# Optimization experiments

Measured on AMD Instinct MI355X. Metric: run time of the kernel, lower is better.

## Reference

```python
import jax, jax.numpy as jnp
import numpy as np

B, T, C = 4, 2048, 1024
N_HEAD = 16
HEAD_DIM = C // N_HEAD


def setup_inputs() -> dict:
    key = jax.random.key(0)
    k1, k2, k3 = jax.random.split(key, 3)
    x = jax.random.normal(k1, (B, T, C), dtype=jnp.float32)
    # torch Linear(n_embd, 3*n_embd, bias=False): weight [out,in]; store transposed [in,out]
    w_qkv = jax.random.normal(k2, (C, 3 * C), dtype=jnp.float32) * (1.0 / np.sqrt(C))
    w_proj = jax.random.normal(k3, (C, C), dtype=jnp.float32) * (1.0 / np.sqrt(C))
    return {"x": x, "w_qkv": w_qkv, "w_proj": w_proj}


def reference(x, w_qkv, w_proj):
    Bb, Tt, Cc = x.shape
    qkv = x @ w_qkv  # [B,T,3C]
    q, k, v = jnp.split(qkv, 3, axis=2)
    # [B,T,H,D] -> [B,H,T,D]
    def heads(t):
        return t.reshape(Bb, Tt, N_HEAD, HEAD_DIM).transpose(0, 2, 1, 3)
    q, k, v = heads(q), heads(k), heads(v)
    att = jnp.einsum("bhqd,bhkd->bhqk", q, k) / jnp.sqrt(jnp.float32(HEAD_DIM))
    causal = jnp.tril(jnp.ones((Tt, Tt), dtype=bool))
    att = jnp.where(causal, att, -jnp.inf)
    att = jax.nn.softmax(att, axis=-1)
    y = jnp.einsum("bhqk,bhkd->bhqd", att, v)  # [B,H,T,D]
    y = y.transpose(0, 2, 1, 3).reshape(Bb, Tt, Cc)
    return y @ w_proj
```

## Files before the change

### kernel.cpp

```cpp
#include <hip/hip_runtime.h>
#include <hip/hip_bf16.h>

typedef unsigned short u16;
typedef __bf16 bf16x8 __attribute__((ext_vector_type(8)));
typedef float f32x4 __attribute__((ext_vector_type(4)));
typedef float f32x16 __attribute__((ext_vector_type(16)));
typedef unsigned short u16x8 __attribute__((ext_vector_type(8)));
typedef unsigned short u16x4 __attribute__((ext_vector_type(4)));
typedef unsigned int u32x4 __attribute__((ext_vector_type(4)));

__device__ __forceinline__ u16 f2bf(float f) {
  unsigned u = __builtin_bit_cast(unsigned, f);
  u += 0x7FFFu + ((u >> 16) & 1u);
  return (u16)(u >> 16);
}

__device__ __forceinline__ unsigned cvt_pk_bf16(float lo, float hi_) {
  unsigned r;
  asm("v_cvt_pk_bf16_f32 %0, %1, %2" : "=v"(r) : "v"(lo), "v"(hi_));
  return r;
}

#define GLD16(gp, lp)                                                          \
  __builtin_amdgcn_global_load_lds(                                            \
      (const __attribute__((address_space(1))) void*)(gp),                     \
      (__attribute__((address_space(3))) void*)(lp), 16, 0, 0)


__global__ __launch_bounds__(256) void cast_f32_bf16(
    const float* __restrict__ in, u16* __restrict__ out, int n4) {
  int i = blockIdx.x * 256 + threadIdx.x;
  if (i >= n4) return;
  float4 v = ((const float4*)in)[i];
  u16x4 o = {f2bf(v.x), f2bf(v.y), f2bf(v.z), f2bf(v.w)};
  *(u16x4*)(out + (size_t)i * 4) = o;
}

__global__ __launch_bounds__(256) void transpose_cast(
    const float* __restrict__ in, u16* __restrict__ out, int R, int C) {
  __shared__ float t[32][33];
  int c0 = blockIdx.x * 32, r0 = blockIdx.y * 32;
  int tx = threadIdx.x, ty = threadIdx.y;
#pragma unroll
  for (int k = 0; k < 4; ++k)
    t[ty + 8 * k][tx] = in[(size_t)(r0 + ty + 8 * k) * C + c0 + tx];
  __syncthreads();
#pragma unroll
  for (int k = 0; k < 4; ++k)
    out[(size_t)(c0 + ty + 8 * k) * R + r0 + tx] = f2bf(t[tx][ty + 8 * k]);
}


template <int EPI>
__global__ __launch_bounds__(256) void gemm_bt(
    const u16* __restrict__ A, const u16* __restrict__ Bt, int K,
    u16* __restrict__ Qd, u16* __restrict__ Kd, u16* __restrict__ Vd,
    float* __restrict__ Od, int N) {
  __shared__ u16 As[128 * 64];
  __shared__ u16 Bs[128 * 64];
  int tid = threadIdx.x;
  int l = tid & 63, w = tid >> 6;
  int wr = w >> 1, wc = w & 1;
  int lr = l & 15, lg = l >> 4;
  int nwg = (int)gridDim.x;
  int bid = (int)blockIdx.x;
  int wg = (bid & 7) * (nwg >> 3) + (bid >> 3);
  int nx = N >> 7;
  int m0 = (wg / nx) * 128, n0 = (wg % nx) * 128;

  f32x4 acc[4][4];
  f32x4 z4 = {0.f, 0.f, 0.f, 0.f};
#pragma unroll
  for (int mi = 0; mi < 4; ++mi)
#pragma unroll
    for (int ni = 0; ni < 4; ++ni) acc[mi][ni] = z4;

  for (int kt = 0; kt < K; kt += 64) {
#pragma unroll
    for (int it = 0; it < 4; ++it) {
      int q = it * 256 + tid;
      int r = q >> 3, s = q & 7;
      int sw = (s ^ (r & 7)) << 3;
      GLD16(A + (size_t)(m0 + r) * K + kt + sw, As + it * 2048 + w * 512);
      GLD16(Bt + (size_t)(n0 + r) * K + kt + sw, Bs + it * 2048 + w * 512);
    }
    __syncthreads();

#pragma unroll
    for (int ks2 = 0; ks2 < 2; ++ks2) {
      bf16x8 af[4], bfv[4];
#pragma unroll
      for (int mi = 0; mi < 4; ++mi) {
        int row = wr * 64 + mi * 16 + lr;
        af[mi] = *(const bf16x8*)&As[row * 64 + (((ks2 * 4 + lg) ^ (row & 7)) << 3)];
      }
#pragma unroll
      for (int ni = 0; ni < 4; ++ni) {
        int col = wc * 64 + ni * 16 + lr;
        bfv[ni] = *(const bf16x8*)&Bs[col * 64 + (((ks2 * 4 + lg) ^ (col & 7)) << 3)];
      }
#pragma unroll
      for (int mi = 0; mi < 4; ++mi)
#pragma unroll
        for (int ni = 0; ni < 4; ++ni)
          acc[mi][ni] = __builtin_amdgcn_mfma_f32_16x16x32_bf16(
              af[mi], bfv[ni], acc[mi][ni], 0, 0, 0);
    }
    __syncthreads();
  }

  if (EPI == 0) {
    int s_blk = n0 >> 10;
    u16* dst = (s_blk == 0) ? Qd : ((s_blk == 1) ? Kd : Vd);
#pragma unroll
    for (int mi = 0; mi < 4; ++mi)
#pragma unroll
      for (int ni = 0; ni < 4; ++ni)
#pragma unroll
        for (int i = 0; i < 4; ++i) {
          int m = m0 + wr * 64 + mi * 16 + lg * 4 + i;
          int n = n0 + wc * 64 + ni * 16 + lr;
          int b = m >> 11, t = m & 2047;
          int c = n & 1023, h = c >> 6, d = c & 63;
          dst[((size_t)(b * 16 + h) * 2048 + t) * 64 + d] = f2bf(acc[mi][ni][i]);
        }
  } else {
#pragma unroll
    for (int mi = 0; mi < 4; ++mi)
#pragma unroll
      for (int ni = 0; ni < 4; ++ni)
#pragma unroll
        for (int i = 0; i < 4; ++i) {
          int m = m0 + wr * 64 + mi * 16 + lg * 4 + i;
          int n = n0 + wc * 64 + ni * 16 + lr;
          Od[(size_t)m * N + n] = acc[mi][ni][i];
        }
  }
}


__global__ __launch_bounds__(128, 3) void attn_fwd(
    const u16* __restrict__ Qg, const u16* __restrict__ Kg,
    const u16* __restrict__ Vg, u16* __restrict__ Yg) {
  __shared__ u16 Ks[2][64 * 64];
  __shared__ u16 Vt[64 * 64];

  int tid = threadIdx.x;
  int l = tid & 63, w = tid >> 6;
  int l31 = l & 31, hi = l >> 5, l7 = l & 7;
  int bid = blockIdx.x;
  int qt = 31 - (bid >> 6);
  int bh = bid & 63;
  const u16* Qb = Qg + (size_t)bh * 131072;
  const u16* Kb = Kg + (size_t)bh * 131072;
  const u16* Vb = Vg + (size_t)bh * 131072;
  int b = bh >> 4, h = bh & 15;

  int t8 = tid >> 3, dq = tid & 7;
  int q0w = qt * 64 + w * 32;
  int jn = qt;

  bf16x8 qreg[4];
#pragma unroll
  for (int ds = 0; ds < 4; ++ds)
    qreg[ds] =
        *(const bf16x8*)(Qb + (size_t)(q0w + l31) * 64 + ds * 16 + hi * 8);

  f32x16 o_acc[2];
#pragma unroll
  for (int dt = 0; dt < 2; ++dt)
#pragma unroll
    for (int r = 0; r < 16; ++r) o_acc[dt][r] = 0.f;
  float m_run = -3e38f, l_run = 0.f;

  u16x8 va[2], vb[2];
#pragma unroll
  for (int it = 0; it < 4; ++it) {
    int r = it * 16 + t8;
    GLD16(Kb + (size_t)r * 64 + ((dq ^ (r & 7)) << 3),
          &Ks[0][it * 1024 + w * 512]);
  }
#pragma unroll
  for (int it = 0; it < 2; ++it) {
    int rr = it * 16 + t8;
    va[it] = *(const u16x8*)(Vb + (size_t)(2 * rr) * 64 + dq * 8);
    vb[it] = *(const u16x8*)(Vb + (size_t)(2 * rr + 1) * 64 + dq * 8);
  }

  for (int j = 0; j <= jn; ++j) {
    int kv0 = j * 64;
    const u16* ksb = Ks[j & 1];
#pragma unroll
    for (int it = 0; it < 2; ++it) {
      int rr = it * 16 + t8;
      int rr2 = (rr & ~6) | ((rr & 2) << 1) | ((rr & 4) >> 1);
#pragma unroll
      for (int jj = 0; jj < 8; ++jj) {
        int d = dq * 8 + jj;
        unsigned wv = (unsigned)va[it][jj] | ((unsigned)vb[it][jj] << 16);
        *(unsigned*)(Vt + d * 64 + (((rr2 >> 2) ^ jj ^ dq) << 3) +
                     ((rr2 & 3) << 1)) = wv;
      }
    }
    __syncthreads();

    if (j < jn) {
      int kv1 = kv0 + 64;
#pragma unroll
      for (int it = 0; it < 4; ++it) {
        int r = it * 16 + t8;
        GLD16(Kb + (size_t)(kv1 + r) * 64 + ((dq ^ (r & 7)) << 3),
              &Ks[(j + 1) & 1][it * 1024 + w * 512]);
      }
#pragma unroll
      for (int it = 0; it < 2; ++it) {
        int rr = it * 16 + t8;
        va[it] = *(const u16x8*)(Vb + (size_t)(kv1 + 2 * rr) * 64 + dq * 8);
        vb[it] = *(const u16x8*)(Vb + (size_t)(kv1 + 2 * rr + 1) * 64 + dq * 8);
      }
    }

    {
      int qg = q0w + l31;
      bf16x8 kf[2][4];
#pragma unroll
      for (int kt = 0; kt < 2; ++kt)
#pragma unroll
        for (int ds = 0; ds < 4; ++ds)
          kf[kt][ds] = *(const bf16x8*)&ksb[(32 * kt + l31) * 64 +
                                            (((2 * ds + hi) ^ l7) << 3)];
      f32x16 sa[2];
      __builtin_amdgcn_s_setprio(1);
#pragma unroll
      for (int kt = 0; kt < 2; ++kt) {
        f32x16 acc;
#pragma unroll
        for (int r = 0; r < 16; ++r) acc[r] = 0.f;
#pragma unroll
        for (int ds = 0; ds < 4; ++ds)
          acc = __builtin_amdgcn_mfma_f32_32x32x16_bf16(kf[kt][ds], qreg[ds],
                                                        acc, 0, 0, 0);
        sa[kt] = acc;
      }
      __builtin_amdgcn_s_setprio(0);

      float mloc = -3e38f;
      if (kv0 + 63 > q0w) {
#pragma unroll
        for (int kt = 0; kt < 2; ++kt)
#pragma unroll
          for (int r = 0; r < 16; ++r) {
            int kg = kv0 + kt * 32 + ((r & 3) + 8 * (r >> 2) + 4 * hi);
            float v = sa[kt][r];
            v = (kg <= qg) ? v : -8e30f;
            sa[kt][r] = v;
            mloc = fmaxf(mloc, v);
          }
      } else {
#pragma unroll
        for (int kt = 0; kt < 2; ++kt)
#pragma unroll
          for (int r = 0; r < 16; ++r) mloc = fmaxf(mloc, sa[kt][r]);
      }
      float mx = fmaxf(mloc, __shfl_xor(mloc, 32)) * 0.125f;
      if (!__all(mx <= m_run + 8.f)) {
        float mn = fmaxf(m_run, mx);
        float fsc = __expf(m_run - mn);
        m_run = mn;
        l_run *= fsc;
#pragma unroll
        for (int r = 0; r < 16; ++r) {
          float fv = __shfl(fsc, (r & 3) + 8 * (r >> 2) + 4 * hi + 32 * hi);
          o_acc[0][r] *= fv;
          o_acc[1][r] *= fv;
        }
      }
      float mm = m_run * 1.44269504f;
      float lloc = 0.f;
#pragma unroll
      for (int kt = 0; kt < 2; ++kt)
#pragma unroll
        for (int r = 0; r < 16; ++r) {
          float p = exp2f(__builtin_fmaf(sa[kt][r], 0.18033688f, -mm));
          sa[kt][r] = p;
          lloc += p;
        }
      l_run += lloc;
      unsigned pk0[8], pk1[8];
#pragma unroll
      for (int m = 0; m < 8; ++m) {
        pk0[m] = cvt_pk_bf16(sa[0][2 * m], sa[0][2 * m + 1]);
        pk1[m] = cvt_pk_bf16(sa[1][2 * m], sa[1][2 * m + 1]);
      }
      bf16x8 vf[2][4];
#pragma unroll
      for (int dt = 0; dt < 2; ++dt)
#pragma unroll
        for (int ks = 0; ks < 4; ++ks) {
          int d = 32 * dt + l31;
          int ch = ((2 * ks + hi) ^ (d & 7) ^ ((d >> 3) & 7)) & 7;
          vf[dt][ks] = *(const bf16x8*)&Vt[d * 64 + (ch << 3)];
        }
#pragma unroll
      for (int ks = 0; ks < 4; ++ks) {
        int c0 = 4 * (ks & 1);
        u32x4 fa;
        fa.x = (ks < 2) ? pk0[c0] : pk1[c0];
        fa.y = (ks < 2) ? pk0[c0 + 1] : pk1[c0 + 1];
        fa.z = (ks < 2) ? pk0[c0 + 2] : pk1[c0 + 2];
        fa.w = (ks < 2) ? pk0[c0 + 3] : pk1[c0 + 3];
        bf16x8 paf = __builtin_bit_cast(bf16x8, fa);
        __builtin_amdgcn_s_setprio(1);
#pragma unroll
        for (int dt = 0; dt < 2; ++dt)
          o_acc[dt] = __builtin_amdgcn_mfma_f32_32x32x16_bf16(
              paf, vf[dt][ks], o_acc[dt], 0, 0, 0);
        __builtin_amdgcn_s_setprio(0);
      }
    }
    __builtin_amdgcn_sched_barrier(0);
    __builtin_amdgcn_s_barrier();
    __builtin_amdgcn_sched_barrier(0);
  }

  l_run += __shfl_xor(l_run, 32);

#pragma unroll
  for (int r = 0; r < 16; ++r) {
    int crow = (r & 3) + 8 * (r >> 2) + 4 * hi;
    float li = __shfl(l_run, crow + 32 * hi);
    float inv = 1.f / li;
    int q = q0w + crow;
#pragma unroll
    for (int dt = 0; dt < 2; ++dt) {
      float y = o_acc[dt][r] * inv;
      Yg[(size_t)(b * 2048 + q) * 1024 + h * 64 + dt * 32 + l31] = f2bf(y);
    }
  }
}


extern "C" void kernel_launch(void* const* d_in, const int* in_sizes, int n_in,
                              void* d_out, int out_size, void* d_ws, size_t ws_size,
                              hipStream_t stream) {
  const float* x = (const float*)d_in[0];
  const float* w_qkv = (const float*)d_in[1];
  const float* w_proj = (const float*)d_in[2];
  float* out = (float*)d_out;
  u16* ws = (u16*)d_ws;

  u16* xb = ws;
  u16* wq = xb + 8388608;
  u16* wp = wq + 3145728;
  u16* Qb = wp + 1048576;
  u16* Kb = Qb + 8388608;
  u16* Vb = Kb + 8388608;
  u16* Yb = xb;

  cast_f32_bf16<<<8192, 256, 0, stream>>>(x, xb, 2097152);
  transpose_cast<<<dim3(96, 32), dim3(32, 8), 0, stream>>>(w_qkv, wq, 1024, 3072);
  transpose_cast<<<dim3(32, 32), dim3(32, 8), 0, stream>>>(w_proj, wp, 1024, 1024);
  gemm_bt<0><<<1536, 256, 0, stream>>>(xb, wq, 1024, Qb, Kb, Vb, nullptr, 3072);
  attn_fwd<<<2048, 128, 0, stream>>>(Qb, Kb, Vb, Yb);
  gemm_bt<1><<<512, 256, 0, stream>>>(Yb, wp, 1024, nullptr, nullptr, nullptr, out, 1024);
}
```

Measured before the change: 174.6 us.

## Triple-buffer GEMM loads with 256x128 tiles and 512-thread blocks

Replaces the single-buffered GEMM main loop with a three-stage LDS ring that prefetches two K-tiles ahead, using explicit vmcnt waits and raw barriers. Doubles the M tile to 256 with eight waves per block and raises wave priority around the MFMA bursts. K is hardcoded to 1024. The aim is to hide global-load latency behind matrix math and cut barrier stalls. The cost is large LDS use, which limits occupancy to one block per CU.

Result: slower. 188.5 us (+8.0%).

```diff
diff --git a/kernel.cpp b/kernel.cpp
--- a/kernel.cpp
+++ b/kernel.cpp
@@ -51,13 +51,64 @@
 }
 
 
+#define G_SYNC(NSTR)                                                           \
+  __builtin_amdgcn_sched_barrier(0);                                           \
+  asm volatile("s_waitcnt vmcnt(" NSTR ")" ::: "memory");                      \
+  __builtin_amdgcn_s_barrier();                                                \
+  __builtin_amdgcn_sched_barrier(0);
+
+#define G_STAGE(U)                                                             \
+  {                                                                            \
+    u16* abase = As + ((U) % 3) * 16384;                                       \
+    u16* bbase = Bs + ((U) % 3) * 8192;                                        \
+    const int kt0 = (U) * 64;                                                  \
+    _Pragma("unroll") for (int it = 0; it < 4; ++it) {                         \
+      int q = it * 512 + tid;                                                  \
+      int r = q >> 3, s = q & 7;                                               \
+      GLD16(A + (size_t)(m0 + r) * 1024 + kt0 + ((s ^ (r & 7)) << 3),          \
+            abase + it * 4096 + w * 512);                                      \
+    }                                                                          \
+    _Pragma("unroll") for (int it = 0; it < 2; ++it) {                         \
+      int q = it * 512 + tid;                                                  \
+      int r = q >> 3, s = q & 7;                                               \
+      GLD16(Bt + (size_t)(n0 + r) * 1024 + kt0 + ((s ^ (r & 7)) << 3),         \
+            bbase + it * 4096 + w * 512);                                      \
+    }                                                                          \
+    __builtin_amdgcn_sched_barrier(0);                                         \
+  }
+
+#define G_COMPUTE(T)                                                           \
+  {                                                                            \
+    const u16* ab = As + ((T) % 3) * 16384;                                    \
+    const u16* bb = Bs + ((T) % 3) * 8192;                                     \
+    _Pragma("unroll") for (int ks2 = 0; ks2 < 2; ++ks2) {                      \
+      bf16x8 af[4], bfv[4];                                                    \
+      _Pragma("unroll") for (int mi = 0; mi < 4; ++mi) {                       \
+        int row = wr * 64 + mi * 16 + lr;                                      \
+        af[mi] =                                                               \
+            *(const bf16x8*)&ab[row * 64 + (((ks2 * 4 + lg) ^ (row & 7)) << 3)];\
+      }                                                                        \
+      _Pragma("unroll") for (int ni = 0; ni < 4; ++ni) {                       \
+        int col = wc * 64 + ni * 16 + lr;                                      \
+        bfv[ni] =                                                              \
+            *(const bf16x8*)&bb[col * 64 + (((ks2 * 4 + lg) ^ (col & 7)) << 3)];\
+      }                                                                        \
+      __builtin_amdgcn_s_setprio(1);                                           \
+      _Pragma("unroll") for (int mi = 0; mi < 4; ++mi)                         \
+          _Pragma("unroll") for (int ni = 0; ni < 4; ++ni)                     \
+              acc[mi][ni] = __builtin_amdgcn_mfma_f32_16x16x32_bf16(           \
+                  af[mi], bfv[ni], acc[mi][ni], 0, 0, 0);                      \
+      __builtin_amdgcn_s_setprio(0);                                           \
+    }                                                                          \
+  }
+
 template <int EPI>
-__global__ __launch_bounds__(256) void gemm_bt(
-    const u16* __restrict__ A, const u16* __restrict__ Bt, int K,
+__global__ __launch_bounds__(512) void gemm_bt(
+    const u16* __restrict__ A, const u16* __restrict__ Bt,
     u16* __restrict__ Qd, u16* __restrict__ Kd, u16* __restrict__ Vd,
     float* __restrict__ Od, int N) {
-  __shared__ u16 As[128 * 64];
-  __shared__ u16 Bs[128 * 64];
+  __shared__ u16 As[3 * 16384];
+  __shared__ u16 Bs[3 * 8192];
   int tid = threadIdx.x;
   int l = tid & 63, w = tid >> 6;
   int wr = w >> 1, wc = w & 1;
@@ -66,7 +117,7 @@
   int bid = (int)blockIdx.x;
   int wg = (bid & 7) * (nwg >> 3) + (bid >> 3);
   int nx = N >> 7;
-  int m0 = (wg / nx) * 128, n0 = (wg % nx) * 128;
+  int m0 = (wg / nx) * 256, n0 = (wg % nx) * 128;
 
   f32x4 acc[4][4];
   f32x4 z4 = {0.f, 0.f, 0.f, 0.f};
@@ -75,39 +126,18 @@
 #pragma unroll
     for (int ni = 0; ni < 4; ++ni) acc[mi][ni] = z4;
 
-  for (int kt = 0; kt < K; kt += 64) {
-#pragma unroll
-    for (int it = 0; it < 4; ++it) {
-      int q = it * 256 + tid;
-      int r = q >> 3, s = q & 7;
-      int sw = (s ^ (r & 7)) << 3;
-      GLD16(A + (size_t)(m0 + r) * K + kt + sw, As + it * 2048 + w * 512);
-      GLD16(Bt + (size_t)(n0 + r) * K + kt + sw, Bs + it * 2048 + w * 512);
-    }
-    __syncthreads();
-
-#pragma unroll
-    for (int ks2 = 0; ks2 < 2; ++ks2) {
-      bf16x8 af[4], bfv[4];
-#pragma unroll
-      for (int mi = 0; mi < 4; ++mi) {
-        int row = wr * 64 + mi * 16 + lr;
-        af[mi] = *(const bf16x8*)&As[row * 64 + (((ks2 * 4 + lg) ^ (row & 7)) << 3)];
-      }
-#pragma unroll
-      for (int ni = 0; ni < 4; ++ni) {
-        int col = wc * 64 + ni * 16 + lr;
-        bfv[ni] = *(const bf16x8*)&Bs[col * 64 + (((ks2 * 4 + lg) ^ (col & 7)) << 3)];
-      }
-#pragma unroll
-      for (int mi = 0; mi < 4; ++mi)
-#pragma unroll
-        for (int ni = 0; ni < 4; ++ni)
-          acc[mi][ni] = __builtin_amdgcn_mfma_f32_16x16x32_bf16(
-              af[mi], bfv[ni], acc[mi][ni], 0, 0, 0);
-    }
-    __syncthreads();
-  }
+  G_STAGE(0)
+  G_STAGE(1)
+#pragma unroll 1
+  for (int t = 0; t < 14; ++t) {
+    G_SYNC("6")
+    G_STAGE(t + 2)
+    G_COMPUTE(t)
+  }
+  G_SYNC("6")
+  G_COMPUTE(14)
+  G_SYNC("0")
+  G_COMPUTE(15)
 
   if (EPI == 0) {
     int s_blk = n0 >> 10;
@@ -360,7 +390,7 @@
   cast_f32_bf16<<<8192, 256, 0, stream>>>(x, xb, 2097152);
   transpose_cast<<<dim3(96, 32), dim3(32, 8), 0, stream>>>(w_qkv, wq, 1024, 3072);
   transpose_cast<<<dim3(32, 32), dim3(32, 8), 0, stream>>>(w_proj, wp, 1024, 1024);
-  gemm_bt<0><<<1536, 256, 0, stream>>>(xb, wq, 1024, Qb, Kb, Vb, nullptr, 3072);
+  gemm_bt<0><<<768, 512, 0, stream>>>(xb, wq, Qb, Kb, Vb, nullptr, 3072);
   attn_fwd<<<2048, 128, 0, stream>>>(Qb, Kb, Vb, Yb);
-  gemm_bt<1><<<512, 256, 0, stream>>>(Yb, wp, 1024, nullptr, nullptr, nullptr, out, 1024);
-}
+  gemm_bt<1><<<256, 512, 0, stream>>>(Yb, wp, nullptr, nullptr, nullptr, out, 1024);
+}
```
